# Optimization experiments

Hardware: AMD Instinct MI355X
Metric: run time of the kernel (lower is better)

## Reference

```python
import jax, jax.numpy as jnp
import numpy as np

N_NODES = 100000


def setup_inputs() -> dict:
    key = jax.random.key(0)
    ks = jax.random.split(key, 6)
    x = jax.random.normal(ks[0], (N_NODES, 3), dtype=jnp.float32)
    edge_index = jax.random.randint(ks[1], (2, 1600000), 0, N_NODES, dtype=jnp.int32)
    W1 = jax.random.normal(ks[2], (6, 64), dtype=jnp.float32) * 0.2
    b1 = jnp.zeros((64,), dtype=jnp.float32)
    W2 = jax.random.normal(ks[3], (67, 128), dtype=jnp.float32) * 0.1
    b2 = jnp.zeros((128,), dtype=jnp.float32)
    Wc = jax.random.normal(ks[4], (128, 5), dtype=jnp.float32) * 0.1
    bc = jnp.zeros((5,), dtype=jnp.float32)
    return {"x": x, "edge_index": edge_index, "W1": W1, "b1": b1,
            "W2": W2, "b2": b2, "Wc": Wc, "bc": bc}


def _pointnet_conv(h, rel, src, dst, W, b, n):
    # gather neighbor features, MLP on [h_j, pos_j - pos_i], max-aggregate per node
    msg = jnp.concatenate([h[src], rel], axis=-1) @ W + b  # [E, out]
    agg = jax.ops.segment_max(msg, dst, num_segments=n)    # [N, out]
    return jax.nn.relu(agg)  # relu also maps -inf (isolated nodes) to 0


def reference(x, edge_index, W1, b1, W2, b2, Wc, bc):
    src, dst = edge_index[0], edge_index[1]
    pos = x  # forward uses data.x for both x and pos
    rel = pos[src] - pos[dst]                       # [E, 3]
    h = _pointnet_conv(x, rel, src, dst, W1, b1, N_NODES)   # [N, 64]
    h = _pointnet_conv(h, rel, src, dst, W2, b2, N_NODES)   # [N, 128]
    logits = h @ Wc + bc                            # [N, 5]
    return jax.nn.log_softmax(logits, axis=-1)
```

## Files before the change

kernel.cpp:

```cpp
#include <hip/hip_runtime.h>
#include <cstdint>

#define CAP 56
#define NBITS 8
#define BINSZ 256
#define BIN_CAP 5120
#define TILE_E 8192
#define SCANN 512

typedef _Float16 h2 __attribute__((ext_vector_type(2)));
typedef _Float16 h4 __attribute__((ext_vector_type(4)));

static __device__ inline h4 pkmax4(h4 a, h4 b) {
#if __has_builtin(__builtin_elementwise_max)
    return __builtin_elementwise_max(a, b);
#else
    h4 r;
    h2 alo = {a.x,a.y}, ahi = {a.z,a.w}, blo = {b.x,b.y}, bhi = {b.z,b.w}, rlo, rhi;
    asm("v_pk_max_f16 %0, %1, %2" : "=v"(rlo) : "v"(alo), "v"(blo));
    asm("v_pk_max_f16 %0, %1, %2" : "=v"(rhi) : "v"(ahi), "v"(bhi));
    r.x=rlo.x; r.y=rlo.y; r.z=rhi.x; r.w=rhi.y;
    return r;
#endif
}

__global__ __launch_bounds__(256) void bin_kernel(
    const int* __restrict__ ei, int* __restrict__ bin_cnt,
    int* __restrict__ pairs, int E, int nbins)
{
    __shared__ int hist[SCANN];
    __shared__ int sc[SCANN];
    __shared__ int gbase[SCANN];
    __shared__ int lofs[SCANN];
    __shared__ int words[TILE_E];
    __shared__ unsigned short binOf[TILE_E];
    int t = threadIdx.x;
    for (int i = t; i < SCANN; i += 256) { hist[i] = 0; lofs[i] = 0; }
    __syncthreads();
    int e0 = blockIdx.x * TILE_E;
    int s[32], d[32];
    #pragma unroll
    for (int i = 0; i < 32; ++i) {
        int e = e0 + t + i * 256;
        bool ok = e < E;
        s[i] = ok ? ei[e] : 0;
        d[i] = ok ? ei[E + e] : -1;
        if (ok) atomicAdd(&hist[d[i] >> NBITS], 1);
    }
    __syncthreads();
    sc[t] = hist[t]; sc[t + 256] = hist[t + 256];
    __syncthreads();
    for (int off = 1; off < SCANN; off <<= 1) {
        int i0 = t, i1 = t + 256;
        int v0 = (i0 >= off) ? sc[i0 - off] : 0;
        int v1 = (i1 >= off) ? sc[i1 - off] : 0;
        __syncthreads();
        sc[i0] += v0; sc[i1] += v1;
        __syncthreads();
    }
    for (int i = t; i < nbins; i += 256)
        gbase[i] = atomicAdd(&bin_cnt[i], hist[i]);
    __syncthreads();
    #pragma unroll
    for (int i = 0; i < 32; ++i) {
        if (d[i] >= 0) {
            int b = d[i] >> NBITS;
            int p = atomicAdd(&lofs[b], 1);
            int slot = (sc[b] - hist[b]) + p;
            words[slot] = s[i] | ((d[i] & (BINSZ - 1)) << 17);
            binOf[slot] = (unsigned short)b;
        }
    }
    __syncthreads();
    int total = sc[nbins - 1];
    for (int i = t; i < total; i += 256) {
        int b = binOf[i];
        int off = gbase[b] + (i - (sc[b] - hist[b]));
        if (off < BIN_CAP) pairs[b * BIN_CAP + off] = words[i];
    }
}

__global__ __launch_bounds__(256) void scatter2_kernel(
    const int* __restrict__ pairs, const int* __restrict__ bin_cnt,
    int* __restrict__ cursor, int* __restrict__ bucket, int N)
{
    __shared__ int cur[BINSZ];
    __shared__ int lbuck[BINSZ * CAP];
    int t = threadIdx.x;
    int b = blockIdx.x;
    for (int i = t; i < BINSZ; i += 256) cur[i] = 0;
    __syncthreads();
    int cnt = min(bin_cnt[b], BIN_CAP);
    const int* pp = pairs + b * BIN_CAP;
    for (int i = t; i < cnt; i += 256) {
        int w = pp[i];
        int p = atomicAdd(&cur[w >> 17], 1);
        if (p < CAP) lbuck[(w >> 17) * CAP + p] = w & 0x1FFFF;
    }
    __syncthreads();
    int nbase = b * BINSZ;
    for (int dl = t; dl < BINSZ; dl += 256) {
        int n = nbase + dl;
        if (n >= N) continue;
        int c = min(cur[dl], CAP);
        int e = (c + 7) & ~7;
        int s0 = (c > 0) ? lbuck[dl * CAP] : 0;
        for (int p = c; p < e; ++p) lbuck[dl * CAP + p] = s0;
        cursor[n] = c;
    }
    __syncthreads();
    int4* dst = (int4*)(bucket + (size_t)nbase * CAP);
    const int4* srcv = (const int4*)lbuck;
    for (int i = t; i < BINSZ * CAP / 4; i += 256) dst[i] = srcv[i];
}

__global__ __launch_bounds__(256) void xpack_kernel(
    const float* __restrict__ x, float4* __restrict__ xp, int N)
{
    int n = blockIdx.x * 256 + threadIdx.x;
    if (n < N) xp[n] = make_float4(x[n*3], x[n*3+1], x[n*3+2], 0.f);
}

__global__ __launch_bounds__(256) void agg1_gemm_kernel(
    const float4* __restrict__ xp, const int* __restrict__ cursor,
    const int* __restrict__ bucket, const float* __restrict__ W1,
    const float* __restrict__ b1, const float* __restrict__ W2,
    const float* __restrict__ b2, h4* __restrict__ u2h, int N)
{
    __shared__ float h1T[64][72];
    int tid = threadIdx.x;
    int n0  = blockIdx.x * 64;
    int sub = tid & 15;
    int ng  = tid >> 4;

    float4 q0 = ((const float4*)(W1 + 0*64))[sub];
    float4 q1 = ((const float4*)(W1 + 1*64))[sub];
    float4 q2 = ((const float4*)(W1 + 2*64))[sub];
    float4 t0 = ((const float4*)(W1 + 3*64))[sub];
    float4 t1 = ((const float4*)(W1 + 4*64))[sub];
    float4 t2 = ((const float4*)(W1 + 5*64))[sub];
    float4 c0 = make_float4(q0.x+t0.x, q0.y+t0.y, q0.z+t0.z, q0.w+t0.w);
    float4 c1 = make_float4(q1.x+t1.x, q1.y+t1.y, q1.z+t1.z, q1.w+t1.w);
    float4 c2 = make_float4(q2.x+t2.x, q2.y+t2.y, q2.z+t2.z, q2.w+t2.w);
    float4 bb = ((const float4*)b1)[sub];

    #pragma unroll
    for (int pass = 0; pass < 4; ++pass) {
        int nl = pass * 16 + ng;
        int n  = n0 + nl;
        float4 m = make_float4(-3e38f, -3e38f, -3e38f, -3e38f);
        int cnt = 0;
        if (n < N) {
            cnt = min(cursor[n], CAP);
            int rounds = (cnt + 7) & ~7;
            const int* brow = bucket + (size_t)n * CAP;
            for (int j0 = 0; j0 < rounds; j0 += 8) {
                int sj[8];
                #pragma unroll
                for (int u = 0; u < 8; ++u) sj[u] = brow[j0 + u];
                float4 xs[8];
                #pragma unroll
                for (int u = 0; u < 8; ++u) xs[u] = xp[sj[u]];
                #pragma unroll
                for (int u = 0; u < 8; ++u) {
                    float4 v;
                    v.x = fmaf(xs[u].x, c0.x, fmaf(xs[u].y, c1.x, xs[u].z * c2.x));
                    v.y = fmaf(xs[u].x, c0.y, fmaf(xs[u].y, c1.y, xs[u].z * c2.y));
                    v.z = fmaf(xs[u].x, c0.z, fmaf(xs[u].y, c1.z, xs[u].z * c2.z));
                    v.w = fmaf(xs[u].x, c0.w, fmaf(xs[u].y, c1.w, xs[u].z * c2.w));
                    m.x = fmaxf(m.x, v.x); m.y = fmaxf(m.y, v.y);
                    m.z = fmaxf(m.z, v.z); m.w = fmaxf(m.w, v.w);
                }
            }
        }
        float4 xd = (n < N) ? xp[n] : make_float4(0.f, 0.f, 0.f, 0.f);
        h1T[4*sub+0][nl] = (cnt > 0) ? fmaxf(m.x + bb.x - (xd.x*t0.x + xd.y*t1.x + xd.z*t2.x), 0.f) : 0.f;
        h1T[4*sub+1][nl] = (cnt > 0) ? fmaxf(m.y + bb.y - (xd.x*t0.y + xd.y*t1.y + xd.z*t2.y), 0.f) : 0.f;
        h1T[4*sub+2][nl] = (cnt > 0) ? fmaxf(m.z + bb.z - (xd.x*t0.z + xd.y*t1.z + xd.z*t2.z), 0.f) : 0.f;
        h1T[4*sub+3][nl] = (cnt > 0) ? fmaxf(m.w + bb.w - (xd.x*t0.w + xd.y*t1.w + xd.z*t2.w), 0.f) : 0.f;
    }
    __syncthreads();

    int fi = tid & 31;
    int ni = tid >> 5;
    float acc[8][4];
    #pragma unroll
    for (int r = 0; r < 8; ++r)
        #pragma unroll
        for (int c = 0; c < 4; ++c) acc[r][c] = 0.f;

    const float4* W2v = (const float4*)W2;
    #pragma unroll 4
    for (int k = 0; k < 64; ++k) {
        float4 w  = W2v[k*32 + fi];
        float4 a0 = *(const float4*)&h1T[k][ni*8];
        float4 a1 = *(const float4*)&h1T[k][ni*8+4];
        float hv[8] = {a0.x,a0.y,a0.z,a0.w,a1.x,a1.y,a1.z,a1.w};
        #pragma unroll
        for (int r = 0; r < 8; ++r) {
            acc[r][0] = fmaf(hv[r], w.x, acc[r][0]);
            acc[r][1] = fmaf(hv[r], w.y, acc[r][1]);
            acc[r][2] = fmaf(hv[r], w.z, acc[r][2]);
            acc[r][3] = fmaf(hv[r], w.w, acc[r][3]);
        }
    }
    float4 bb2 = ((const float4*)b2)[fi];
    float4 wa = W2v[64*32 + fi], wb = W2v[65*32 + fi], wc = W2v[66*32 + fi];
    #pragma unroll
    for (int r = 0; r < 8; ++r) {
        int n = n0 + ni*8 + r;
        if (n >= N) break;
        float4 xd = xp[n];
        h4 o4;
        o4.x = (_Float16)(acc[r][0] + bb2.x + xd.x*wa.x + xd.y*wb.x + xd.z*wc.x);
        o4.y = (_Float16)(acc[r][1] + bb2.y + xd.x*wa.y + xd.y*wb.y + xd.z*wc.y);
        o4.z = (_Float16)(acc[r][2] + bb2.z + xd.x*wa.z + xd.y*wb.z + xd.z*wc.z);
        o4.w = (_Float16)(acc[r][3] + bb2.w + xd.x*wa.w + xd.y*wb.w + xd.z*wc.w);
        u2h[(size_t)n * 32 + fi] = o4;
    }
}

__global__ __launch_bounds__(256) void agg2_head_kernel(
    const float* __restrict__ x, const int* __restrict__ cursor,
    const int* __restrict__ bucket, const float* __restrict__ W2,
    const h4* __restrict__ u2v, const float* __restrict__ Wc,
    const float* __restrict__ bc, float* __restrict__ out, int N)
{
    int gid = blockIdx.x * 256 + threadIdx.x;
    int n   = gid >> 5;
    int sub = threadIdx.x & 31;
    if (n >= N) return;
    int cnt = min(cursor[n], CAP);
    int rounds = (cnt + 7) & ~7;
    const int* brow = bucket + (size_t)n * CAP;
    const _Float16 NEG = (_Float16)(-60000.0f);
    h4 hm = { NEG, NEG, NEG, NEG };
    for (int j0 = 0; j0 < rounds; j0 += 8) {
        h4 vv[8];
        #pragma unroll
        for (int u = 0; u < 8; ++u)
            vv[u] = u2v[(size_t)brow[j0+u] * 32 + sub];
        #pragma unroll
        for (int u = 0; u < 8; ++u) hm = pkmax4(hm, vv[u]);
    }
    float4 wa = ((const float4*)(W2 + 64*128))[sub];
    float4 wb = ((const float4*)(W2 + 65*128))[sub];
    float4 wc = ((const float4*)(W2 + 66*128))[sub];
    float x0 = x[n*3], x1 = x[n*3+1], x2 = x[n*3+2];
    float hh0 = (cnt > 0) ? fmaxf((float)hm.x - (x0*wa.x + x1*wb.x + x2*wc.x), 0.f) : 0.f;
    float hh1 = (cnt > 0) ? fmaxf((float)hm.y - (x0*wa.y + x1*wb.y + x2*wc.y), 0.f) : 0.f;
    float hh2 = (cnt > 0) ? fmaxf((float)hm.z - (x0*wa.z + x1*wb.z + x2*wc.z), 0.f) : 0.f;
    float hh3 = (cnt > 0) ? fmaxf((float)hm.w - (x0*wa.w + x1*wb.w + x2*wc.w), 0.f) : 0.f;

    int g = sub * 4;
    float l0 = hh0*Wc[g*5+0] + hh1*Wc[(g+1)*5+0] + hh2*Wc[(g+2)*5+0] + hh3*Wc[(g+3)*5+0];
    float l1 = hh0*Wc[g*5+1] + hh1*Wc[(g+1)*5+1] + hh2*Wc[(g+2)*5+1] + hh3*Wc[(g+3)*5+1];
    float l2 = hh0*Wc[g*5+2] + hh1*Wc[(g+1)*5+2] + hh2*Wc[(g+2)*5+2] + hh3*Wc[(g+3)*5+2];
    float l3 = hh0*Wc[g*5+3] + hh1*Wc[(g+1)*5+3] + hh2*Wc[(g+2)*5+3] + hh3*Wc[(g+3)*5+3];
    float l4 = hh0*Wc[g*5+4] + hh1*Wc[(g+1)*5+4] + hh2*Wc[(g+2)*5+4] + hh3*Wc[(g+3)*5+4];
    #pragma unroll
    for (int off = 16; off > 0; off >>= 1) {
        l0 += __shfl_xor(l0, off);
        l1 += __shfl_xor(l1, off);
        l2 += __shfl_xor(l2, off);
        l3 += __shfl_xor(l3, off);
        l4 += __shfl_xor(l4, off);
    }
    l0 += bc[0]; l1 += bc[1]; l2 += bc[2]; l3 += bc[3]; l4 += bc[4];
    float mx  = fmaxf(fmaxf(fmaxf(l0, l1), fmaxf(l2, l3)), l4);
    float s   = expf(l0-mx) + expf(l1-mx) + expf(l2-mx) + expf(l3-mx) + expf(l4-mx);
    float lse = mx + logf(s);
    if (sub < 5) {
        float v = (sub == 0) ? l0 : (sub == 1) ? l1 : (sub == 2) ? l2
                : (sub == 3) ? l3 : l4;
        out[n*5 + sub] = v - lse;
    }
}

extern "C" void kernel_launch(void* const* d_in, const int* in_sizes, int n_in,
                              void* d_out, int out_size, void* d_ws, size_t ws_size,
                              hipStream_t stream)
{
    const float* x  = (const float*)d_in[0];
    const int*   ei = (const int*)d_in[1];
    const float* W1 = (const float*)d_in[2];
    const float* b1 = (const float*)d_in[3];
    const float* W2 = (const float*)d_in[4];
    const float* b2 = (const float*)d_in[5];
    const float* Wc = (const float*)d_in[6];
    const float* bc = (const float*)d_in[7];
    float* out = (float*)d_out;

    int N = in_sizes[0] / 3;
    int E = in_sizes[1] / 2;
    int nbins = (N + BINSZ - 1) / BINSZ;

    char* ws = (char*)d_ws;
    h4*     u2h     = (h4*)    (ws);
    float4* xp      = (float4*)(ws + 25600000);
    int*    pairs   = (int*)   (ws + 27200000);
    int*    bucket  = (int*)   (ws + 35250000);
    int*    cursor  = (int*)   (ws + 57700000);
    int*    bin_cnt = (int*)   (ws + 58200000);

    (void)hipMemsetAsync(bin_cnt, 0, 2048, stream);

    xpack_kernel<<<(N + 255) / 256, 256, 0, stream>>>(x, xp, N);
    bin_kernel<<<(E + TILE_E - 1) / TILE_E, 256, 0, stream>>>(
        ei, bin_cnt, pairs, E, nbins);
    scatter2_kernel<<<nbins, 256, 0, stream>>>(pairs, bin_cnt, cursor, bucket, N);

    agg1_gemm_kernel<<<(N + 63) / 64, 256, 0, stream>>>(
        xp, cursor, bucket, W1, b1, W2, b2, u2h, N);
    agg2_head_kernel<<<(N * 32 + 255) / 256, 256, 0, stream>>>(
        x, cursor, bucket, W2, u2h, Wc, bc, out, N);
}
```

Before: 231.2 us.

## Widen agg2 gathers to 16-byte half8 loads and prefetch neighbor indices as int4

The second aggregation now maps 16 lanes per node, each gathering 8 fp16 features with a 16-byte load, and the shuffle reduction shrinks to 16 lanes. Both aggregation kernels load neighbor indices as int4 vectors and prefetch the next round's indices while the current gathers run. The bin counter memset is folded into the xpack kernel, saving one launch, and the redundant CAP clamp is removed. The prefetch reads slightly past each node's row, which relies on slack in the workspace.

```diff
diff --git a/kernel.cpp b/kernel.cpp
--- a/kernel.cpp
+++ b/kernel.cpp
@@ -10,16 +10,19 @@
 
 typedef _Float16 h2 __attribute__((ext_vector_type(2)));
 typedef _Float16 h4 __attribute__((ext_vector_type(4)));
-
-static __device__ inline h4 pkmax4(h4 a, h4 b) {
+typedef _Float16 h8 __attribute__((ext_vector_type(8)));
+
+static __device__ inline h8 pkmax8(h8 a, h8 b) {
 #if __has_builtin(__builtin_elementwise_max)
     return __builtin_elementwise_max(a, b);
 #else
-    h4 r;
-    h2 alo = {a.x,a.y}, ahi = {a.z,a.w}, blo = {b.x,b.y}, bhi = {b.z,b.w}, rlo, rhi;
-    asm("v_pk_max_f16 %0, %1, %2" : "=v"(rlo) : "v"(alo), "v"(blo));
-    asm("v_pk_max_f16 %0, %1, %2" : "=v"(rhi) : "v"(ahi), "v"(bhi));
-    r.x=rlo.x; r.y=rlo.y; r.z=rhi.x; r.w=rhi.y;
+    h8 r;
+    #pragma unroll
+    for (int i = 0; i < 8; i += 2) {
+        h2 aa = { a[i], a[i+1] }, bb = { b[i], b[i+1] }, rr;
+        asm("v_pk_max_f16 %0, %1, %2" : "=v"(rr) : "v"(aa), "v"(bb));
+        r[i] = rr.x; r[i+1] = rr.y;
+    }
     return r;
 #endif
 }
@@ -115,10 +118,15 @@
 }
 
 __global__ __launch_bounds__(256) void xpack_kernel(
-    const float* __restrict__ x, float4* __restrict__ xp, int N)
+    const float* __restrict__ x, float4* __restrict__ xp,
+    int* __restrict__ bin_cnt, int N)
 {
     int n = blockIdx.x * 256 + threadIdx.x;
     if (n < N) xp[n] = make_float4(x[n*3], x[n*3+1], x[n*3+2], 0.f);
+    if (blockIdx.x == 0) {
+        bin_cnt[threadIdx.x] = 0;
+        bin_cnt[threadIdx.x + 256] = 0;
+    }
 }
 
 __global__ __launch_bounds__(256) void agg1_gemm_kernel(
@@ -151,16 +159,16 @@
         float4 m = make_float4(-3e38f, -3e38f, -3e38f, -3e38f);
         int cnt = 0;
         if (n < N) {
-            cnt = min(cursor[n], CAP);
+            cnt = cursor[n];
             int rounds = (cnt + 7) & ~7;
-            const int* brow = bucket + (size_t)n * CAP;
+            const int4* brow4 = (const int4*)(bucket + (size_t)n * CAP);
+            int4 ia = brow4[0], ib = brow4[1];
             for (int j0 = 0; j0 < rounds; j0 += 8) {
-                int sj[8];
-                #pragma unroll
-                for (int u = 0; u < 8; ++u) sj[u] = brow[j0 + u];
+                int4 na = brow4[(j0 >> 2) + 2];
+                int4 nb = brow4[(j0 >> 2) + 3];
                 float4 xs[8];
-                #pragma unroll
-                for (int u = 0; u < 8; ++u) xs[u] = xp[sj[u]];
+                xs[0] = xp[ia.x]; xs[1] = xp[ia.y]; xs[2] = xp[ia.z]; xs[3] = xp[ia.w];
+                xs[4] = xp[ib.x]; xs[5] = xp[ib.y]; xs[6] = xp[ib.z]; xs[7] = xp[ib.w];
                 #pragma unroll
                 for (int u = 0; u < 8; ++u) {
                     float4 v;
@@ -171,6 +179,7 @@
                     m.x = fmaxf(m.x, v.x); m.y = fmaxf(m.y, v.y);
                     m.z = fmaxf(m.z, v.z); m.w = fmaxf(m.w, v.w);
                 }
+                ia = na; ib = nb;
             }
         }
         float4 xd = (n < N) ? xp[n] : make_float4(0.f, 0.f, 0.f, 0.f);
@@ -223,43 +232,63 @@
 __global__ __launch_bounds__(256) void agg2_head_kernel(
     const float* __restrict__ x, const int* __restrict__ cursor,
     const int* __restrict__ bucket, const float* __restrict__ W2,
-    const h4* __restrict__ u2v, const float* __restrict__ Wc,
+    const h8* __restrict__ u2v, const float* __restrict__ Wc,
     const float* __restrict__ bc, float* __restrict__ out, int N)
 {
     int gid = blockIdx.x * 256 + threadIdx.x;
-    int n   = gid >> 5;
-    int sub = threadIdx.x & 31;
+    int n   = gid >> 4;
+    int sub = threadIdx.x & 15;
     if (n >= N) return;
-    int cnt = min(cursor[n], CAP);
+    int cnt = cursor[n];
     int rounds = (cnt + 7) & ~7;
-    const int* brow = bucket + (size_t)n * CAP;
+    const int4* brow4 = (const int4*)(bucket + (size_t)n * CAP);
     const _Float16 NEG = (_Float16)(-60000.0f);
-    h4 hm = { NEG, NEG, NEG, NEG };
+    h8 hm = { NEG, NEG, NEG, NEG, NEG, NEG, NEG, NEG };
+    int4 ia = brow4[0], ib = brow4[1];
     for (int j0 = 0; j0 < rounds; j0 += 8) {
-        h4 vv[8];
-        #pragma unroll
-        for (int u = 0; u < 8; ++u)
-            vv[u] = u2v[(size_t)brow[j0+u] * 32 + sub];
-        #pragma unroll
-        for (int u = 0; u < 8; ++u) hm = pkmax4(hm, vv[u]);
-    }
-    float4 wa = ((const float4*)(W2 + 64*128))[sub];
-    float4 wb = ((const float4*)(W2 + 65*128))[sub];
-    float4 wc = ((const float4*)(W2 + 66*128))[sub];
+        int4 na = brow4[(j0 >> 2) + 2];
+        int4 nb = brow4[(j0 >> 2) + 3];
+        h8 v0 = u2v[(size_t)ia.x * 16 + sub];
+        h8 v1 = u2v[(size_t)ia.y * 16 + sub];
+        h8 v2 = u2v[(size_t)ia.z * 16 + sub];
+        h8 v3 = u2v[(size_t)ia.w * 16 + sub];
+        h8 v4 = u2v[(size_t)ib.x * 16 + sub];
+        h8 v5 = u2v[(size_t)ib.y * 16 + sub];
+        h8 v6 = u2v[(size_t)ib.z * 16 + sub];
+        h8 v7 = u2v[(size_t)ib.w * 16 + sub];
+        hm = pkmax8(hm, v0); hm = pkmax8(hm, v1);
+        hm = pkmax8(hm, v2); hm = pkmax8(hm, v3);
+        hm = pkmax8(hm, v4); hm = pkmax8(hm, v5);
+        hm = pkmax8(hm, v6); hm = pkmax8(hm, v7);
+        ia = na; ib = nb;
+    }
+    const float4* W2v = (const float4*)W2;
+    float4 wa0 = W2v[64*32 + sub*2], wa1 = W2v[64*32 + sub*2 + 1];
+    float4 wb0 = W2v[65*32 + sub*2], wb1 = W2v[65*32 + sub*2 + 1];
+    float4 wc0 = W2v[66*32 + sub*2], wc1 = W2v[66*32 + sub*2 + 1];
     float x0 = x[n*3], x1 = x[n*3+1], x2 = x[n*3+2];
-    float hh0 = (cnt > 0) ? fmaxf((float)hm.x - (x0*wa.x + x1*wb.x + x2*wc.x), 0.f) : 0.f;
-    float hh1 = (cnt > 0) ? fmaxf((float)hm.y - (x0*wa.y + x1*wb.y + x2*wc.y), 0.f) : 0.f;
-    float hh2 = (cnt > 0) ? fmaxf((float)hm.z - (x0*wa.z + x1*wb.z + x2*wc.z), 0.f) : 0.f;
-    float hh3 = (cnt > 0) ? fmaxf((float)hm.w - (x0*wa.w + x1*wb.w + x2*wc.w), 0.f) : 0.f;
-
-    int g = sub * 4;
-    float l0 = hh0*Wc[g*5+0] + hh1*Wc[(g+1)*5+0] + hh2*Wc[(g+2)*5+0] + hh3*Wc[(g+3)*5+0];
-    float l1 = hh0*Wc[g*5+1] + hh1*Wc[(g+1)*5+1] + hh2*Wc[(g+2)*5+1] + hh3*Wc[(g+3)*5+1];
-    float l2 = hh0*Wc[g*5+2] + hh1*Wc[(g+1)*5+2] + hh2*Wc[(g+2)*5+2] + hh3*Wc[(g+3)*5+2];
-    float l3 = hh0*Wc[g*5+3] + hh1*Wc[(g+1)*5+3] + hh2*Wc[(g+2)*5+3] + hh3*Wc[(g+3)*5+3];
-    float l4 = hh0*Wc[g*5+4] + hh1*Wc[(g+1)*5+4] + hh2*Wc[(g+2)*5+4] + hh3*Wc[(g+3)*5+4];
-    #pragma unroll
-    for (int off = 16; off > 0; off >>= 1) {
+    float hh[8];
+    hh[0] = (cnt > 0) ? fmaxf((float)hm[0] - (x0*wa0.x + x1*wb0.x + x2*wc0.x), 0.f) : 0.f;
+    hh[1] = (cnt > 0) ? fmaxf((float)hm[1] - (x0*wa0.y + x1*wb0.y + x2*wc0.y), 0.f) : 0.f;
+    hh[2] = (cnt > 0) ? fmaxf((float)hm[2] - (x0*wa0.z + x1*wb0.z + x2*wc0.z), 0.f) : 0.f;
+    hh[3] = (cnt > 0) ? fmaxf((float)hm[3] - (x0*wa0.w + x1*wb0.w + x2*wc0.w), 0.f) : 0.f;
+    hh[4] = (cnt > 0) ? fmaxf((float)hm[4] - (x0*wa1.x + x1*wb1.x + x2*wc1.x), 0.f) : 0.f;
+    hh[5] = (cnt > 0) ? fmaxf((float)hm[5] - (x0*wa1.y + x1*wb1.y + x2*wc1.y), 0.f) : 0.f;
+    hh[6] = (cnt > 0) ? fmaxf((float)hm[6] - (x0*wa1.z + x1*wb1.z + x2*wc1.z), 0.f) : 0.f;
+    hh[7] = (cnt > 0) ? fmaxf((float)hm[7] - (x0*wa1.w + x1*wb1.w + x2*wc1.w), 0.f) : 0.f;
+
+    int g = sub * 8;
+    float l0 = 0.f, l1 = 0.f, l2 = 0.f, l3 = 0.f, l4 = 0.f;
+    #pragma unroll
+    for (int k = 0; k < 8; ++k) {
+        l0 = fmaf(hh[k], Wc[(g+k)*5+0], l0);
+        l1 = fmaf(hh[k], Wc[(g+k)*5+1], l1);
+        l2 = fmaf(hh[k], Wc[(g+k)*5+2], l2);
+        l3 = fmaf(hh[k], Wc[(g+k)*5+3], l3);
+        l4 = fmaf(hh[k], Wc[(g+k)*5+4], l4);
+    }
+    #pragma unroll
+    for (int off = 8; off > 0; off >>= 1) {
         l0 += __shfl_xor(l0, off);
         l1 += __shfl_xor(l1, off);
         l2 += __shfl_xor(l2, off);
@@ -303,15 +332,13 @@
     int*    cursor  = (int*)   (ws + 57700000);
     int*    bin_cnt = (int*)   (ws + 58200000);
 
-    (void)hipMemsetAsync(bin_cnt, 0, 2048, stream);
-
-    xpack_kernel<<<(N + 255) / 256, 256, 0, stream>>>(x, xp, N);
+    xpack_kernel<<<(N + 255) / 256, 256, 0, stream>>>(x, xp, bin_cnt, N);
     bin_kernel<<<(E + TILE_E - 1) / TILE_E, 256, 0, stream>>>(
         ei, bin_cnt, pairs, E, nbins);
     scatter2_kernel<<<nbins, 256, 0, stream>>>(pairs, bin_cnt, cursor, bucket, N);
 
     agg1_gemm_kernel<<<(N + 63) / 64, 256, 0, stream>>>(
         xp, cursor, bucket, W1, b1, W2, b2, u2h, N);
-    agg2_head_kernel<<<(N * 32 + 255) / 256, 256, 0, stream>>>(
-        x, cursor, bucket, W2, u2h, Wc, bc, out, N);
-}
+    agg2_head_kernel<<<(N * 16 + 255) / 256, 256, 0, stream>>>(
+        x, cursor, bucket, W2, (const h8*)u2h, Wc, bc, out, N);
+}
```

Result: faster. 224.0 us (-3.1%).
